# Kernel optimization log

Hardware: AMD Instinct MI355X
Metric: run time of the kernel (lower is better)

Reference implementation:

```python
import jax, jax.numpy as jnp
import numpy as np

N_NODES = 10000
N_GRAPHS = 64
IN_DIM = 256
HID = 256
N_CLASSES = 10
N_EDGES = 320000


def _gcn_conv(x, W, b, src, dst):
    # PyG GCNConv: h = x @ W; add self-loops (weight 1); symmetric norm D^-1/2 (A+I) D^-1/2; aggregate; + b
    N = x.shape[0]
    h = x @ W  # [N, H]
    loops = jnp.arange(N, dtype=src.dtype)
    s = jnp.concatenate([src, loops])
    d = jnp.concatenate([dst, loops])
    w = jnp.ones(s.shape[0], dtype=x.dtype)
    deg = jax.ops.segment_sum(w, d, num_segments=N)
    dinv = jnp.where(deg > 0, jax.lax.rsqrt(jnp.maximum(deg, 1.0)), 0.0)
    norm = dinv[s] * dinv[d]  # [E+N]
    msg = h[s] * norm[:, None]  # gather + scale
    out = jax.ops.segment_sum(msg, d, num_segments=N)  # scatter-add
    return out + b


def setup_inputs() -> dict:
    key = jax.random.key(0)
    ks = jax.random.split(key, 12)
    x = jax.random.normal(ks[0], (N_NODES, IN_DIM), dtype=jnp.float32)
    edge_index = jax.random.randint(ks[1], (2, N_EDGES), 0, N_NODES, dtype=jnp.int64)
    batch = jnp.sort(jax.random.randint(ks[2], (N_NODES,), 0, N_GRAPHS, dtype=jnp.int64))
    g = 1.0 / np.sqrt(IN_DIM)
    W1 = jax.random.uniform(ks[3], (IN_DIM, HID), jnp.float32, -g, g)
    b1 = jnp.zeros((HID,), jnp.float32)
    gh = 1.0 / np.sqrt(HID)
    W2 = jax.random.uniform(ks[4], (HID, HID), jnp.float32, -gh, gh)
    b2 = jnp.zeros((HID,), jnp.float32)
    W3 = jax.random.uniform(ks[5], (HID, HID), jnp.float32, -gh, gh)
    b3 = jnp.zeros((HID,), jnp.float32)
    Wlin = jax.random.uniform(ks[6], (HID, N_CLASSES), jnp.float32, -gh, gh)
    blin = jax.random.uniform(ks[7], (N_CLASSES,), jnp.float32, -gh, gh)
    return {"x": x, "W1": W1, "b1": b1, "W2": W2, "b2": b2, "W3": W3, "b3": b3,
            "Wlin": Wlin, "blin": blin, "edge_index": edge_index, "batch": batch}


def reference(x, W1, b1, W2, b2, W3, b3, Wlin, blin, edge_index, batch):
    src, dst = edge_index[0], edge_index[1]
    h = jax.nn.relu(_gcn_conv(x, W1, b1, src, dst))
    h = jax.nn.relu(_gcn_conv(h, W2, b2, src, dst))
    h = jax.nn.relu(_gcn_conv(h, W3, b3, src, dst))
    # global mean pool over graphs (dropout is identity in eval mode)
    sums = jax.ops.segment_sum(h, batch, num_segments=N_GRAPHS)  # [G, H]
    cnts = jax.ops.segment_sum(jnp.ones((h.shape[0],), h.dtype), batch, num_segments=N_GRAPHS)
    pooled = sums / jnp.maximum(cnts, 1.0)[:, None]
    logits = pooled @ Wlin + blin
    return jax.nn.log_softmax(logits, axis=-1)
```

## Files before the change

kernel.cpp:

```cpp
#include <hip/hip_runtime.h>
#include <hip/hip_bf16.h>
#include <math.h>

#define HIDDEN 256
#define NCLS 10

typedef __attribute__((ext_vector_type(8))) short short8;
typedef __attribute__((ext_vector_type(4))) float f32x4;

static __device__ __forceinline__ float bf16lo(unsigned u) {
    return __uint_as_float((u & 0xffffu) << 16);
}
static __device__ __forceinline__ float bf16hi(unsigned u) {
    return __uint_as_float(u & 0xffff0000u);
}
static __device__ __forceinline__ unsigned short f2bf(float f) {
    unsigned x = __float_as_uint(f);
    x += 0x7fffu + ((x >> 16) & 1u);
    return (unsigned short)(x >> 16);
}
static __device__ __forceinline__ unsigned pack2(float lo, float hi) {
    return (unsigned)f2bf(lo) | ((unsigned)f2bf(hi) << 16);
}

static __device__ __forceinline__ void fma8(float* acc, uint4 u, float w) {
    acc[0] = fmaf(bf16lo(u.x), w, acc[0]);
    acc[1] = fmaf(bf16hi(u.x), w, acc[1]);
    acc[2] = fmaf(bf16lo(u.y), w, acc[2]);
    acc[3] = fmaf(bf16hi(u.y), w, acc[3]);
    acc[4] = fmaf(bf16lo(u.z), w, acc[4]);
    acc[5] = fmaf(bf16hi(u.z), w, acc[5]);
    acc[6] = fmaf(bf16lo(u.w), w, acc[6]);
    acc[7] = fmaf(bf16hi(u.w), w, acc[7]);
}

__global__ void k_count(const int* __restrict__ dst, int* __restrict__ ecnt, int E) {
    int e = blockIdx.x * blockDim.x + threadIdx.x;
    if (e < E) atomicAdd(&ecnt[dst[e]], 1);
}

__global__ __launch_bounds__(1024) void k_scan(const int* __restrict__ ecnt,
                                               int* __restrict__ rowstart,
                                               int* __restrict__ cursor,
                                               float* __restrict__ dinv, int N, int E) {
    __shared__ int sums[1024];
    int t = threadIdx.x;
    const int CH = (N + 1023) / 1024;
    int base = t * CH;
    int local = 0;
    for (int i = 0; i < CH; ++i) {
        int idx = base + i;
        if (idx < N) local += ecnt[idx];
    }
    sums[t] = local;
    __syncthreads();
    for (int off = 1; off < 1024; off <<= 1) {
        int v = (t >= off) ? sums[t - off] : 0;
        __syncthreads();
        sums[t] += v;
        __syncthreads();
    }
    int run = (t == 0) ? 0 : sums[t - 1];
    for (int i = 0; i < CH; ++i) {
        int idx = base + i;
        if (idx < N) {
            rowstart[idx] = run;
            cursor[idx] = run;
            dinv[idx] = rsqrtf((float)(ecnt[idx] + 1));
            run += ecnt[idx];
        }
    }
    if (t == 0) rowstart[N] = E;
}

__global__ void k_fill(const int* __restrict__ src, const int* __restrict__ dst,
                       const float* __restrict__ dinv, int* __restrict__ cursor,
                       uint2* __restrict__ csr, int E) {
    int e = blockIdx.x * blockDim.x + threadIdx.x;
    if (e < E) {
        int d = dst[e];
        int s = src[e];
        int pos = atomicAdd(&cursor[d], 1);
        uint2 ent;
        ent.x = (unsigned)s;
        ent.y = __float_as_uint(dinv[s] * dinv[d]);
        csr[pos] = ent;
    }
}

__global__ __launch_bounds__(256) void k_prep(const float* __restrict__ x,
                                              unsigned* __restrict__ x16,
                                              const float* __restrict__ W1,
                                              const float* __restrict__ W2,
                                              const float* __restrict__ W3,
                                              short8* __restrict__ P1,
                                              short8* __restrict__ P2,
                                              short8* __restrict__ P3,
                                              int n4, int nb_cvt) {
    const int b = blockIdx.x;
    if (b < nb_cvt) {
        int i = b * 256 + threadIdx.x;
        if (i < n4) {
            float4 v = reinterpret_cast<const float4*>(x)[i];
            uint2 o;
            o.x = pack2(v.x, v.y);
            o.y = pack2(v.z, v.w);
            reinterpret_cast<uint2*>(x16)[i] = o;
        }
    } else {
        int pb = b - nb_cvt;
        int which = pb >> 5;
        int id = (pb & 31) * 256 + threadIdx.x;
        const float* W = (which == 0) ? W1 : (which == 1) ? W2 : W3;
        short8* P = (which == 0) ? P1 : (which == 1) ? P2 : P3;
        int l = id & 63;
        int tt = (id >> 6) & 15;
        int s = id >> 10;
        int col = tt * 16 + (l & 15);
        int k0 = s * 32 + (l >> 4) * 8;
        short8 v;
#pragma unroll
        for (int j = 0; j < 8; ++j)
            v[j] = (short)f2bf(W[(size_t)(k0 + j) * HIDDEN + col]);
        P[id] = v;
    }
}

__global__ __launch_bounds__(256) void k_gemm(const unsigned short* __restrict__ A,
                                              const short8* __restrict__ P,
                                              unsigned short* __restrict__ C) {
    const int l = threadIdx.x & 63;
    const int w = threadIdx.x >> 6;
    const int g = l >> 4;
    const int r = l & 15;
    const int mwave = blockIdx.x * 64 + w * 16;
    const int nb = blockIdx.y * 8;

    f32x4 acc[8] = {};
    const unsigned short* arow = A + (size_t)(mwave + r) * HIDDEN;

#pragma unroll
    for (int s = 0; s < 8; ++s) {
        short8 a = *reinterpret_cast<const short8*>(arow + s * 32 + g * 8);
#pragma unroll
        for (int f = 0; f < 8; ++f) {
            short8 bfrag = P[(s * 16 + nb + f) * 64 + l];
            acc[f] = __builtin_amdgcn_mfma_f32_16x16x32_bf16(a, bfrag, acc[f], 0, 0, 0);
        }
    }
#pragma unroll
    for (int f = 0; f < 8; ++f) {
        int col = blockIdx.y * 128 + f * 16 + r;
#pragma unroll
        for (int q = 0; q < 4; ++q) {
            int row = mwave + g * 4 + q;
            C[(size_t)row * HIDDEN + col] = f2bf(acc[f][q]);
        }
    }
}

__global__ __launch_bounds__(256) void k_agg(const unsigned* __restrict__ H,
                                             const uint2* __restrict__ csr,
                                             const int* __restrict__ rowstart,
                                             const float* __restrict__ dinv,
                                             const float* __restrict__ bias,
                                             unsigned* __restrict__ out, int N) {
    const int n = blockIdx.x * 4 + (threadIdx.x >> 6);
    if (n >= N) return;
    const int l = threadIdx.x & 63;
    const int q = l & 31;
    const int h = l >> 5;
    const uint4* __restrict__ H4 = reinterpret_cast<const uint4*>(H);

    float acc[8] = {0.f, 0.f, 0.f, 0.f, 0.f, 0.f, 0.f, 0.f};
    if (h == 0) {
        const float di = dinv[n];
        fma8(acc, H4[(size_t)n * 32 + q], di * di);
    }

    int e = rowstart[n];
    const int e1 = rowstart[n + 1];
    for (; e + 8 <= e1; e += 8) {
        int bx = e + 4 * h;
        uint2 ed0 = csr[bx + 0];
        uint2 ed1 = csr[bx + 1];
        uint2 ed2 = csr[bx + 2];
        uint2 ed3 = csr[bx + 3];
        uint4 r0 = H4[(size_t)ed0.x * 32 + q];
        uint4 r1 = H4[(size_t)ed1.x * 32 + q];
        uint4 r2 = H4[(size_t)ed2.x * 32 + q];
        uint4 r3 = H4[(size_t)ed3.x * 32 + q];
        fma8(acc, r0, __uint_as_float(ed0.y));
        fma8(acc, r1, __uint_as_float(ed1.y));
        fma8(acc, r2, __uint_as_float(ed2.y));
        fma8(acc, r3, __uint_as_float(ed3.y));
    }
    for (int te = e + h; te < e1; te += 2) {
        uint2 ed = csr[te];
        uint4 r0 = H4[(size_t)ed.x * 32 + q];
        fma8(acc, r0, __uint_as_float(ed.y));
    }

#pragma unroll
    for (int j = 0; j < 8; ++j) acc[j] += __shfl_xor(acc[j], 32);

    if (h == 0) {
        const float4* __restrict__ b4 = reinterpret_cast<const float4*>(bias);
        float4 ba = b4[q * 2];
        float4 bb = b4[q * 2 + 1];
        uint4 o;
        o.x = pack2(fmaxf(acc[0] + ba.x, 0.f), fmaxf(acc[1] + ba.y, 0.f));
        o.y = pack2(fmaxf(acc[2] + ba.z, 0.f), fmaxf(acc[3] + ba.w, 0.f));
        o.z = pack2(fmaxf(acc[4] + bb.x, 0.f), fmaxf(acc[5] + bb.y, 0.f));
        o.w = pack2(fmaxf(acc[6] + bb.z, 0.f), fmaxf(acc[7] + bb.w, 0.f));
        reinterpret_cast<uint4*>(out)[(size_t)n * 32 + q] = o;
    }
}

__device__ __forceinline__ int lower_bound_i(const int* a, int n, int val) {
    int lo = 0, hi = n;
    while (lo < hi) {
        int mid = (lo + hi) >> 1;
        if (a[mid] < val) lo = mid + 1; else hi = mid;
    }
    return lo;
}

__global__ __launch_bounds__(128) void k_pool_part(const unsigned* __restrict__ H,
                                                   const int* __restrict__ batch,
                                                   float* __restrict__ partial, int N) {
    const int g = blockIdx.x;
    const int s = blockIdx.y;
    const int p = threadIdx.x;
    const int lo = lower_bound_i(batch, N, g);
    const int hi = lower_bound_i(batch, N, g + 1);
    float sx = 0.f, sy = 0.f;
    for (int n = lo + s; n < hi; n += 8) {
        unsigned u = H[(size_t)n * 128 + p];
        sx += bf16lo(u);
        sy += bf16hi(u);
    }
    float2 v; v.x = sx; v.y = sy;
    reinterpret_cast<float2*>(partial)[(size_t)(g * 8 + s) * 128 + p] = v;
}

__global__ __launch_bounds__(256) void k_cls(const float* __restrict__ partial,
                                             const int* __restrict__ batch,
                                             const float* __restrict__ Wlin,
                                             const float* __restrict__ blin,
                                             float* __restrict__ out, int N) {
    __shared__ float part[NCLS][HIDDEN];
    const int g = blockIdx.x;
    const int t = threadIdx.x;
    const int lo = lower_bound_i(batch, N, g);
    const int hi = lower_bound_i(batch, N, g + 1);
    float p = 0.f;
#pragma unroll
    for (int s = 0; s < 8; ++s) p += partial[(size_t)(g * 8 + s) * HIDDEN + t];
    p /= fmaxf((float)(hi - lo), 1.f);
#pragma unroll
    for (int c = 0; c < NCLS; ++c) part[c][t] = p * Wlin[(size_t)t * NCLS + c];
    __syncthreads();
    for (int off = 128; off >= 1; off >>= 1) {
        if (t < off) {
#pragma unroll
            for (int c = 0; c < NCLS; ++c) part[c][t] += part[c][t + off];
        }
        __syncthreads();
    }
    if (t == 0) {
        float lg[NCLS];
        float m = -INFINITY;
#pragma unroll
        for (int c = 0; c < NCLS; ++c) {
            lg[c] = part[c][0] + blin[c];
            m = fmaxf(m, lg[c]);
        }
        float se = 0.f;
#pragma unroll
        for (int c = 0; c < NCLS; ++c) se += expf(lg[c] - m);
        float lse = m + logf(se);
#pragma unroll
        for (int c = 0; c < NCLS; ++c) out[(size_t)g * NCLS + c] = lg[c] - lse;
    }
}


extern "C" void kernel_launch(void* const* d_in, const int* in_sizes, int n_in,
                              void* d_out, int out_size, void* d_ws, size_t ws_size,
                              hipStream_t stream) {
    const float* x    = (const float*)d_in[0];
    const float* W1   = (const float*)d_in[1];
    const float* b1   = (const float*)d_in[2];
    const float* W2   = (const float*)d_in[3];
    const float* b2   = (const float*)d_in[4];
    const float* W3   = (const float*)d_in[5];
    const float* b3   = (const float*)d_in[6];
    const float* Wlin = (const float*)d_in[7];
    const float* blin = (const float*)d_in[8];
    const int*   eidx = (const int*)d_in[9];
    const int*   batch= (const int*)d_in[10];
    float* out = (float*)d_out;

    const int N = in_sizes[0] / HIDDEN;
    const int E = in_sizes[9] / 2;
    const int G = out_size / NCLS;
    const int Mp = (N + 63) & ~63;

    const int* src = eidx;
    const int* dst = eidx + E;

    char* base = (char*)d_ws;
    size_t off = 0;
    auto alloc = [&](size_t bytes) -> void* {
        void* p = base + off;
        off = (off + bytes + 255) & ~(size_t)255;
        return p;
    };
    int*      ecnt     = (int*)     alloc((size_t)N * sizeof(int));
    int*      cursor   = (int*)     alloc((size_t)N * sizeof(int));
    float*    dinv     = (float*)   alloc((size_t)N * sizeof(float));
    int*      rowstart = (int*)     alloc((size_t)(N + 1) * sizeof(int));
    uint2*    csr      = (uint2*)   alloc((size_t)E * sizeof(uint2));
    unsigned* x16      = (unsigned*)alloc((size_t)Mp * 128 * sizeof(unsigned));
    unsigned* hA       = (unsigned*)alloc((size_t)Mp * 128 * sizeof(unsigned));
    unsigned* hB       = (unsigned*)alloc((size_t)Mp * 128 * sizeof(unsigned));
    short8*   Wp1      = (short8*)  alloc((size_t)8192 * sizeof(short8));
    short8*   Wp2      = (short8*)  alloc((size_t)8192 * sizeof(short8));
    short8*   Wp3      = (short8*)  alloc((size_t)8192 * sizeof(short8));
    float*    partial  = (float*)   alloc((size_t)G * 8 * HIDDEN * sizeof(float));
    (void)ws_size;

    const int T = 256;
    hipMemsetAsync(ecnt, 0, (size_t)N * sizeof(int), stream);
    k_count<<<(E + T - 1) / T, T, 0, stream>>>(dst, ecnt, E);
    k_scan <<<1, 1024, 0, stream>>>(ecnt, rowstart, cursor, dinv, N, E);
    k_fill <<<(E + T - 1) / T, T, 0, stream>>>(src, dst, dinv, cursor, csr, E);

    const int n4 = N * HIDDEN / 4;
    const int nb_cvt = (n4 + 255) / 256;
    k_prep<<<nb_cvt + 96, 256, 0, stream>>>(x, x16, W1, W2, W3, Wp1, Wp2, Wp3, n4, nb_cvt);

    const dim3 ggrid(Mp / 64, 2);
    const int agg_blocks = (N + 3) / 4;
    k_gemm<<<ggrid, 256, 0, stream>>>((const unsigned short*)x16, Wp1, (unsigned short*)hA);
    k_agg <<<agg_blocks, 256, 0, stream>>>(hA, csr, rowstart, dinv, b1, hB, N);
    k_gemm<<<ggrid, 256, 0, stream>>>((const unsigned short*)hB, Wp2, (unsigned short*)hA);
    k_agg <<<agg_blocks, 256, 0, stream>>>(hA, csr, rowstart, dinv, b2, hB, N);
    k_gemm<<<ggrid, 256, 0, stream>>>((const unsigned short*)hB, Wp3, (unsigned short*)hA);
    k_agg <<<agg_blocks, 256, 0, stream>>>(hA, csr, rowstart, dinv, b3, hB, N);
    k_pool_part<<<dim3(G, 8), 128, 0, stream>>>(hB, batch, partial, N);
    k_cls <<<G, 256, 0, stream>>>(partial, batch, Wlin, blin, out, N);
}
```

Baseline: 182.3 us.

## Fuse CSR build with prep/GEMM launches, narrow GEMM tiles, software-pipeline aggregation

Merges the edge-count kernel with the x/weight bf16 conversion, and the CSR fill with the first layer GEMM, into single launches using block-index dispatch. This removes two launches and lets independent work overlap. The GEMM tile is halved in N, from 128 to 64 columns, which gives a 4-wide grid and more blocks. The aggregation loop is software-pipelined to prefetch the next edge batch's indices and rows before doing the current FMAs, and the CSR buffer is padded by 16 entries so the prefetch reads stay in bounds.

```diff
diff --git a/kernel.cpp b/kernel.cpp
--- a/kernel.cpp
+++ b/kernel.cpp
@@ -34,9 +34,47 @@
     acc[7] = fmaf(bf16hi(u.w), w, acc[7]);
 }
 
-__global__ void k_count(const int* __restrict__ dst, int* __restrict__ ecnt, int E) {
-    int e = blockIdx.x * blockDim.x + threadIdx.x;
-    if (e < E) atomicAdd(&ecnt[dst[e]], 1);
+__global__ __launch_bounds__(256) void k_count_prep(const int* __restrict__ dst,
+                                                    int* __restrict__ ecnt, int E,
+                                                    const float* __restrict__ x,
+                                                    unsigned* __restrict__ x16,
+                                                    const float* __restrict__ W1,
+                                                    const float* __restrict__ W2,
+                                                    const float* __restrict__ W3,
+                                                    short8* __restrict__ P1,
+                                                    short8* __restrict__ P2,
+                                                    short8* __restrict__ P3,
+                                                    int n4, int nbCount, int nb_cvt) {
+    const int b = blockIdx.x;
+    if (b < nbCount) {
+        int e = b * 256 + threadIdx.x;
+        if (e < E) atomicAdd(&ecnt[dst[e]], 1);
+    } else if (b < nbCount + nb_cvt) {
+        int i = (b - nbCount) * 256 + threadIdx.x;
+        if (i < n4) {
+            float4 v = reinterpret_cast<const float4*>(x)[i];
+            uint2 o;
+            o.x = pack2(v.x, v.y);
+            o.y = pack2(v.z, v.w);
+            reinterpret_cast<uint2*>(x16)[i] = o;
+        }
+    } else {
+        int pb = b - nbCount - nb_cvt;
+        int which = pb >> 5;
+        int id = (pb & 31) * 256 + threadIdx.x;
+        const float* W = (which == 0) ? W1 : (which == 1) ? W2 : W3;
+        short8* P = (which == 0) ? P1 : (which == 1) ? P2 : P3;
+        int l = id & 63;
+        int tt = (id >> 6) & 15;
+        int s = id >> 10;
+        int col = tt * 16 + (l & 15);
+        int k0 = s * 32 + (l >> 4) * 8;
+        short8 v;
+#pragma unroll
+        for (int j = 0; j < 8; ++j)
+            v[j] = (short)f2bf(W[(size_t)(k0 + j) * HIDDEN + col]);
+        P[id] = v;
+    }
 }
 
 __global__ __launch_bounds__(1024) void k_scan(const int* __restrict__ ecnt,
@@ -73,89 +111,70 @@
     if (t == 0) rowstart[N] = E;
 }
 
-__global__ void k_fill(const int* __restrict__ src, const int* __restrict__ dst,
-                       const float* __restrict__ dinv, int* __restrict__ cursor,
-                       uint2* __restrict__ csr, int E) {
-    int e = blockIdx.x * blockDim.x + threadIdx.x;
-    if (e < E) {
-        int d = dst[e];
-        int s = src[e];
-        int pos = atomicAdd(&cursor[d], 1);
-        uint2 ent;
-        ent.x = (unsigned)s;
-        ent.y = __float_as_uint(dinv[s] * dinv[d]);
-        csr[pos] = ent;
-    }
-}
-
-__global__ __launch_bounds__(256) void k_prep(const float* __restrict__ x,
-                                              unsigned* __restrict__ x16,
-                                              const float* __restrict__ W1,
-                                              const float* __restrict__ W2,
-                                              const float* __restrict__ W3,
-                                              short8* __restrict__ P1,
-                                              short8* __restrict__ P2,
-                                              short8* __restrict__ P3,
-                                              int n4, int nb_cvt) {
-    const int b = blockIdx.x;
-    if (b < nb_cvt) {
-        int i = b * 256 + threadIdx.x;
-        if (i < n4) {
-            float4 v = reinterpret_cast<const float4*>(x)[i];
-            uint2 o;
-            o.x = pack2(v.x, v.y);
-            o.y = pack2(v.z, v.w);
-            reinterpret_cast<uint2*>(x16)[i] = o;
-        }
-    } else {
-        int pb = b - nb_cvt;
-        int which = pb >> 5;
-        int id = (pb & 31) * 256 + threadIdx.x;
-        const float* W = (which == 0) ? W1 : (which == 1) ? W2 : W3;
-        short8* P = (which == 0) ? P1 : (which == 1) ? P2 : P3;
-        int l = id & 63;
-        int tt = (id >> 6) & 15;
-        int s = id >> 10;
-        int col = tt * 16 + (l & 15);
-        int k0 = s * 32 + (l >> 4) * 8;
-        short8 v;
-#pragma unroll
-        for (int j = 0; j < 8; ++j)
-            v[j] = (short)f2bf(W[(size_t)(k0 + j) * HIDDEN + col]);
-        P[id] = v;
+static __device__ __forceinline__ void gemm_body(const unsigned short* __restrict__ A,
+                                                 const short8* __restrict__ P,
+                                                 unsigned short* __restrict__ C,
+                                                 int bx, int by, int tid) {
+    const int l = tid & 63;
+    const int w = tid >> 6;
+    const int g = l >> 4;
+    const int r = l & 15;
+    const int mwave = bx * 64 + w * 16;
+    const int nb = by * 4;
+
+    f32x4 acc[4] = {};
+    const unsigned short* arow = A + (size_t)(mwave + r) * HIDDEN;
+
+#pragma unroll
+    for (int s = 0; s < 8; ++s) {
+        short8 a = *reinterpret_cast<const short8*>(arow + s * 32 + g * 8);
+#pragma unroll
+        for (int f = 0; f < 4; ++f) {
+            short8 bfrag = P[(s * 16 + nb + f) * 64 + l];
+            acc[f] = __builtin_amdgcn_mfma_f32_16x16x32_bf16(a, bfrag, acc[f], 0, 0, 0);
+        }
+    }
+#pragma unroll
+    for (int f = 0; f < 4; ++f) {
+        int col = by * 64 + f * 16 + r;
+#pragma unroll
+        for (int q = 0; q < 4; ++q) {
+            int row = mwave + g * 4 + q;
+            C[(size_t)row * HIDDEN + col] = f2bf(acc[f][q]);
+        }
     }
 }
 
 __global__ __launch_bounds__(256) void k_gemm(const unsigned short* __restrict__ A,
                                               const short8* __restrict__ P,
                                               unsigned short* __restrict__ C) {
-    const int l = threadIdx.x & 63;
-    const int w = threadIdx.x >> 6;
-    const int g = l >> 4;
-    const int r = l & 15;
-    const int mwave = blockIdx.x * 64 + w * 16;
-    const int nb = blockIdx.y * 8;
-
-    f32x4 acc[8] = {};
-    const unsigned short* arow = A + (size_t)(mwave + r) * HIDDEN;
-
-#pragma unroll
-    for (int s = 0; s < 8; ++s) {
-        short8 a = *reinterpret_cast<const short8*>(arow + s * 32 + g * 8);
-#pragma unroll
-        for (int f = 0; f < 8; ++f) {
-            short8 bfrag = P[(s * 16 + nb + f) * 64 + l];
-            acc[f] = __builtin_amdgcn_mfma_f32_16x16x32_bf16(a, bfrag, acc[f], 0, 0, 0);
-        }
-    }
-#pragma unroll
-    for (int f = 0; f < 8; ++f) {
-        int col = blockIdx.y * 128 + f * 16 + r;
-#pragma unroll
-        for (int q = 0; q < 4; ++q) {
-            int row = mwave + g * 4 + q;
-            C[(size_t)row * HIDDEN + col] = f2bf(acc[f][q]);
-        }
+    gemm_body(A, P, C, blockIdx.x, blockIdx.y, threadIdx.x);
+}
+
+__global__ __launch_bounds__(256) void k_fill_gemm1(const int* __restrict__ src,
+                                                    const int* __restrict__ dst,
+                                                    const float* __restrict__ dinv,
+                                                    int* __restrict__ cursor,
+                                                    uint2* __restrict__ csr, int E,
+                                                    const unsigned short* __restrict__ A,
+                                                    const short8* __restrict__ P,
+                                                    unsigned short* __restrict__ C,
+                                                    int nbFill) {
+    const int b = blockIdx.x;
+    if (b < nbFill) {
+        int e = b * 256 + threadIdx.x;
+        if (e < E) {
+            int d = dst[e];
+            int s = src[e];
+            int pos = atomicAdd(&cursor[d], 1);
+            uint2 ent;
+            ent.x = (unsigned)s;
+            ent.y = __float_as_uint(dinv[s] * dinv[d]);
+            csr[pos] = ent;
+        }
+    } else {
+        int gb = b - nbFill;
+        gemm_body(A, P, C, gb >> 2, gb & 3, threadIdx.x);
     }
 }
 
@@ -178,27 +197,41 @@
         fma8(acc, H4[(size_t)n * 32 + q], di * di);
     }
 
-    int e = rowstart[n];
-    const int e1 = rowstart[n + 1];
-    for (; e + 8 <= e1; e += 8) {
-        int bx = e + 4 * h;
-        uint2 ed0 = csr[bx + 0];
-        uint2 ed1 = csr[bx + 1];
-        uint2 ed2 = csr[bx + 2];
-        uint2 ed3 = csr[bx + 3];
-        uint4 r0 = H4[(size_t)ed0.x * 32 + q];
-        uint4 r1 = H4[(size_t)ed1.x * 32 + q];
-        uint4 r2 = H4[(size_t)ed2.x * 32 + q];
-        uint4 r3 = H4[(size_t)ed3.x * 32 + q];
-        fma8(acc, r0, __uint_as_float(ed0.y));
-        fma8(acc, r1, __uint_as_float(ed1.y));
-        fma8(acc, r2, __uint_as_float(ed2.y));
-        fma8(acc, r3, __uint_as_float(ed3.y));
-    }
-    for (int te = e + h; te < e1; te += 2) {
-        uint2 ed = csr[te];
-        uint4 r0 = H4[(size_t)ed.x * 32 + q];
-        fma8(acc, r0, __uint_as_float(ed.y));
+    const int base = rowstart[n];
+    const int e1   = rowstart[n + 1];
+    const int nfull = (e1 - base) >> 3;
+    const uint2* cp = csr + base + 4 * h;
+
+    if (nfull > 0) {
+        uint2 dA0 = cp[0], dA1 = cp[1], dA2 = cp[2], dA3 = cp[3];
+        uint4 rA0 = H4[(size_t)dA0.x * 32 + q];
+        uint4 rA1 = H4[(size_t)dA1.x * 32 + q];
+        uint4 rA2 = H4[(size_t)dA2.x * 32 + q];
+        uint4 rA3 = H4[(size_t)dA3.x * 32 + q];
+        uint2 dB0 = cp[8], dB1 = cp[9], dB2 = cp[10], dB3 = cp[11];
+        for (int it = 0; it + 1 < nfull; ++it) {
+            cp += 8;
+            uint4 rB0 = H4[(size_t)dB0.x * 32 + q];
+            uint4 rB1 = H4[(size_t)dB1.x * 32 + q];
+            uint4 rB2 = H4[(size_t)dB2.x * 32 + q];
+            uint4 rB3 = H4[(size_t)dB3.x * 32 + q];
+            uint2 dC0 = cp[8], dC1 = cp[9], dC2 = cp[10], dC3 = cp[11];
+            fma8(acc, rA0, __uint_as_float(dA0.y));
+            fma8(acc, rA1, __uint_as_float(dA1.y));
+            fma8(acc, rA2, __uint_as_float(dA2.y));
+            fma8(acc, rA3, __uint_as_float(dA3.y));
+            dA0 = dB0; dA1 = dB1; dA2 = dB2; dA3 = dB3;
+            dB0 = dC0; dB1 = dC1; dB2 = dC2; dB3 = dC3;
+            rA0 = rB0; rA1 = rB1; rA2 = rB2; rA3 = rB3;
+        }
+        fma8(acc, rA0, __uint_as_float(dA0.y));
+        fma8(acc, rA1, __uint_as_float(dA1.y));
+        fma8(acc, rA2, __uint_as_float(dA2.y));
+        fma8(acc, rA3, __uint_as_float(dA3.y));
+    }
+    for (int e = base + 8 * nfull + h; e < e1; e += 2) {
+        uint2 ed = csr[e];
+        fma8(acc, H4[(size_t)ed.x * 32 + q], __uint_as_float(ed.y));
     }
 
 #pragma unroll
@@ -321,7 +354,7 @@
     int*      cursor   = (int*)     alloc((size_t)N * sizeof(int));
     float*    dinv     = (float*)   alloc((size_t)N * sizeof(float));
     int*      rowstart = (int*)     alloc((size_t)(N + 1) * sizeof(int));
-    uint2*    csr      = (uint2*)   alloc((size_t)E * sizeof(uint2));
+    uint2*    csr      = (uint2*)   alloc((size_t)(E + 16) * sizeof(uint2));
     unsigned* x16      = (unsigned*)alloc((size_t)Mp * 128 * sizeof(unsigned));
     unsigned* hA       = (unsigned*)alloc((size_t)Mp * 128 * sizeof(unsigned));
     unsigned* hB       = (unsigned*)alloc((size_t)Mp * 128 * sizeof(unsigned));
@@ -331,19 +364,22 @@
     float*    partial  = (float*)   alloc((size_t)G * 8 * HIDDEN * sizeof(float));
     (void)ws_size;
 
-    const int T = 256;
-    hipMemsetAsync(ecnt, 0, (size_t)N * sizeof(int), stream);
-    k_count<<<(E + T - 1) / T, T, 0, stream>>>(dst, ecnt, E);
-    k_scan <<<1, 1024, 0, stream>>>(ecnt, rowstart, cursor, dinv, N, E);
-    k_fill <<<(E + T - 1) / T, T, 0, stream>>>(src, dst, dinv, cursor, csr, E);
-
+    const int nbCount = (E + 255) / 256;
     const int n4 = N * HIDDEN / 4;
     const int nb_cvt = (n4 + 255) / 256;
-    k_prep<<<nb_cvt + 96, 256, 0, stream>>>(x, x16, W1, W2, W3, Wp1, Wp2, Wp3, n4, nb_cvt);
-
-    const dim3 ggrid(Mp / 64, 2);
+    hipMemsetAsync(ecnt, 0, (size_t)N * sizeof(int), stream);
+    k_count_prep<<<nbCount + nb_cvt + 96, 256, 0, stream>>>(
+        dst, ecnt, E, x, x16, W1, W2, W3, Wp1, Wp2, Wp3, n4, nbCount, nb_cvt);
+    k_scan<<<1, 1024, 0, stream>>>(ecnt, rowstart, cursor, dinv, N, E);
+
+    const int nbFill = (E + 255) / 256;
+    const int gemmBlocks = (Mp / 64) * 4;
+    k_fill_gemm1<<<nbFill + gemmBlocks, 256, 0, stream>>>(
+        src, dst, dinv, cursor, csr, E,
+        (const unsigned short*)x16, Wp1, (unsigned short*)hA, nbFill);
+
+    const dim3 ggrid(Mp / 64, 4);
     const int agg_blocks = (N + 3) / 4;
-    k_gemm<<<ggrid, 256, 0, stream>>>((const unsigned short*)x16, Wp1, (unsigned short*)hA);
     k_agg <<<agg_blocks, 256, 0, stream>>>(hA, csr, rowstart, dinv, b1, hB, N);
     k_gemm<<<ggrid, 256, 0, stream>>>((const unsigned short*)hB, Wp2, (unsigned short*)hA);
     k_agg <<<agg_blocks, 256, 0, stream>>>(hA, csr, rowstart, dinv, b2, hB, N);
```

Result: faster. 166.2 us (-8.8%).
